# Kernel tuning notes

Measured on AMD Instinct MI355X. Metric: run time of the kernel, lower is better.

## Reference

```python
import jax, jax.numpy as jnp
import numpy as np

LN_EPS = 1e-12
NEG_INF = -1e9


def setup_inputs() -> dict:
    key = jax.random.key(0)
    ks = jax.random.split(key, 4)
    B, S, H = 8, 2048, 1024
    inputs = jax.random.normal(ks[0], (B, S, H), dtype=jnp.float32)
    masks = jnp.ones((B, S), dtype=jnp.int32)
    scale = 1.0 / np.sqrt(H)
    Wq = jax.random.normal(ks[1], (H, H), dtype=jnp.float32) * scale
    bq = jnp.zeros((H,), dtype=jnp.float32)
    Wk = jax.random.normal(ks[2], (H, H), dtype=jnp.float32) * scale
    bk = jnp.zeros((H,), dtype=jnp.float32)
    ln_gamma = jnp.ones((H,), dtype=jnp.float32)
    ln_beta = jnp.zeros((H,), dtype=jnp.float32)
    return {"inputs": inputs, "masks": masks, "Wq": Wq, "bq": bq,
            "Wk": Wk, "bk": bk, "ln_gamma": ln_gamma, "ln_beta": ln_beta}


def _layernorm(x, gamma, beta):
    mu = jnp.mean(x, axis=-1, keepdims=True)
    var = jnp.mean(jnp.square(x - mu), axis=-1, keepdims=True)
    return (x - mu) * jax.lax.rsqrt(var + LN_EPS) * gamma + beta


def reference(inputs, masks, Wq, bq, Wk, bk, ln_gamma, ln_beta):
    # inputs: [B,S,H]; masks: [B,S] (1 = keep key position)
    H = inputs.shape[-1]
    query = inputs @ Wq + bq                      # [B,S,H]
    key_ = inputs @ Wk + bk                       # [B,S,H]
    scores = jnp.einsum('bqh,bkh->bqk', query, key_) * (1.0 / jnp.sqrt(jnp.float32(H)))
    # logits_mask: invalid key positions get large negative logit
    scores = jnp.where(masks[:, None, :] != 0, scores, NEG_INF)
    probs = jax.nn.softmax(scores, axis=-1)       # [B,S,S]
    context = jnp.einsum('bqk,bkh->bqh', probs, inputs)  # value = raw inputs
    return _layernorm(inputs + context, ln_gamma, ln_beta)
```

## Files before the change

### kernel.cpp

```cpp
#include <hip/hip_runtime.h>
#include <stdint.h>
#include <stddef.h>

typedef _Float16 f16_t;
typedef _Float16 f16x8 __attribute__((ext_vector_type(8)));
typedef _Float16 f16x4 __attribute__((ext_vector_type(4)));
typedef float    f32x4 __attribute__((ext_vector_type(4)));

#define AS_G __attribute__((address_space(1)))
#define AS_L __attribute__((address_space(3)))

__device__ __forceinline__ void gload_lds16(const void* g, void* l) {
  __builtin_amdgcn_global_load_lds((const AS_G uint32_t*)g, (AS_L uint32_t*)l, 16, 0, 0);
}

#define LN_EPS 1e-12f

__global__ __launch_bounds__(256) void cast_f16_kernel(const float* __restrict__ in,
                                                       f16_t* __restrict__ out) {
  int i = blockIdx.x * 256 + threadIdx.x;
  float4 v = ((const float4*)in)[i];
  f16x4 o = {(f16_t)v.x, (f16_t)v.y, (f16_t)v.z, (f16_t)v.w};
  ((f16x4*)out)[i] = o;
}

__global__ __launch_bounds__(256) void xprep_kernel(const float* __restrict__ in,
                                                    f16_t* __restrict__ xb,
                                                    f16_t* __restrict__ xt) {
  __shared__ float tile[32][33];
  int b = blockIdx.z;
  const float* inb = in + (size_t)b * 2048 * 1024;
  f16_t* xbb = xb + (size_t)b * 2048 * 1024;
  f16_t* xtb = xt + (size_t)b * 1024 * 2048;
  int tx = threadIdx.x, ty = threadIdx.y;
  int c0 = blockIdx.x * 32, r0 = blockIdx.y * 32;
#pragma unroll
  for (int i = 0; i < 32; i += 8) {
    float v = inb[(size_t)(r0 + ty + i) * 1024 + (c0 + tx)];
    tile[ty + i][tx] = v;
    xbb[(size_t)(r0 + ty + i) * 1024 + (c0 + tx)] = (f16_t)v;
  }
  __syncthreads();
#pragma unroll
  for (int i = 0; i < 32; i += 8)
    xtb[(size_t)(c0 + ty + i) * 2048 + (r0 + tx)] = (f16_t)tile[tx][ty + i];
}

__global__ __launch_bounds__(256) void wvec_kernel(const float* __restrict__ Wq,
                                                   const float* __restrict__ bq,
                                                   const float* __restrict__ Wk,
                                                   const float* __restrict__ bk,
                                                   float* __restrict__ wqbk,
                                                   float* __restrict__ wkbq,
                                                   float* __restrict__ c0) {
  __shared__ float red[4];
  int bid = blockIdx.x, tid = threadIdx.x;
  const float* rowp; const float* vecp; float* outp;
  if (bid < 1024)      { rowp = Wq + (size_t)bid * 1024; vecp = bk; outp = wqbk + bid; }
  else if (bid < 2048) { rowp = Wk + (size_t)(bid - 1024) * 1024; vecp = bq; outp = wkbq + (bid - 1024); }
  else                 { rowp = bq; vecp = bk; outp = c0; }
  float4 a = ((const float4*)rowp)[tid];
  float4 b = ((const float4*)vecp)[tid];
  float s = a.x * b.x + a.y * b.y + a.z * b.z + a.w * b.w;
#pragma unroll
  for (int off = 32; off > 0; off >>= 1) s += __shfl_xor(s, off, 64);
  if ((tid & 63) == 0) red[tid >> 6] = s;
  __syncthreads();
  if (tid == 0) *outp = red[0] + red[1] + red[2] + red[3];
}

__global__ __launch_bounds__(256) void cqck_kernel(const float* __restrict__ X,
                                                   const float* __restrict__ wqbk,
                                                   const float* __restrict__ wkbq,
                                                   float* __restrict__ cq,
                                                   float* __restrict__ ck) {
  __shared__ float r1[4], r2[4];
  int m = blockIdx.x, tid = threadIdx.x;
  float4 x = ((const float4*)(X + (size_t)m * 1024))[tid];
  float4 a = ((const float4*)wqbk)[tid];
  float4 b = ((const float4*)wkbq)[tid];
  float s1 = x.x * a.x + x.y * a.y + x.z * a.z + x.w * a.w;
  float s2 = x.x * b.x + x.y * b.y + x.z * b.z + x.w * b.w;
#pragma unroll
  for (int off = 32; off > 0; off >>= 1) { s1 += __shfl_xor(s1, off, 64); s2 += __shfl_xor(s2, off, 64); }
  if ((tid & 63) == 0) { r1[tid >> 6] = s1; r2[tid >> 6] = s2; }
  __syncthreads();
  if (tid == 0) {
    cq[m] = r1[0] + r1[1] + r1[2] + r1[3];
    ck[m] = r2[0] + r2[1] + r2[2] + r2[3];
  }
}

__global__ __launch_bounds__(256) void gemm_bt_kernel(
    const f16_t* __restrict__ A, const f16_t* __restrict__ Bt, f16_t* __restrict__ C,
    const float* __restrict__ cq, const float* __restrict__ ck, const float* __restrict__ c0p,
    const int* __restrict__ mask, const float* __restrict__ invl, float* __restrict__ lpart,
    int lda, int ldb, int ldc, int K, float scale, int mode,
    size_t sA, size_t sB, size_t sC) {
  __shared__ f16_t As[2][128 * 64];
  __shared__ f16_t Bs[2][128 * 64];

  const int tid = threadIdx.x;
  const int lane = tid & 63;
  const int wv = tid >> 6;
  const int m16 = lane & 15;
  const int quad = lane >> 4;
  const int wr = (wv >> 1) * 64;
  const int wc = (wv & 1) * 64;

  const f16_t* Ab = A + blockIdx.z * sA + (size_t)blockIdx.x * 128 * lda;
  const f16_t* Bb = Bt + blockIdx.z * sB + (size_t)blockIdx.y * 128 * ldb;

  const int lr8 = lane >> 3;
  const int ch8 = (lane & 7) ^ lr8;
  const f16_t* gA[4]; const f16_t* gB[4];
  f16_t* lA[4]; f16_t* lB[4];
#pragma unroll
  for (int j = 0; j < 4; ++j) {
    int row = wv * 32 + j * 8 + lr8;
    gA[j] = Ab + (size_t)row * lda + ch8 * 8;
    gB[j] = Bb + (size_t)row * ldb + ch8 * 8;
    lA[j] = &As[0][(wv * 32 + j * 8) * 64];
    lB[j] = &Bs[0][(wv * 32 + j * 8) * 64];
  }

  int aoff[4], boff[4], swz[2];
#pragma unroll
  for (int t = 0; t < 4; ++t) {
    aoff[t] = (wr + t * 16 + m16) * 64;
    boff[t] = (wc + t * 16 + m16) * 64;
  }
#pragma unroll
  for (int s = 0; s < 2; ++s)
    swz[s] = (((s << 2) | quad) ^ (m16 & 7)) * 8;

  f32x4 acc[4][4] = {};

#define STAGE(BUF, KOFF)                                       \
  _Pragma("unroll")                                            \
  for (int j = 0; j < 4; ++j) {                                \
    gload_lds16(gA[j] + (KOFF), lA[j] + (BUF) * (128 * 64));   \
    gload_lds16(gB[j] + (KOFF), lB[j] + (BUF) * (128 * 64));   \
  }

#define COMPUTE(BUF)                                                           \
  _Pragma("unroll")                                                            \
  for (int s = 0; s < 2; ++s) {                                                \
    f16x8 af[4], bfr[4];                                                       \
    _Pragma("unroll")                                                          \
    for (int t = 0; t < 4; ++t) {                                              \
      af[t]  = *(const f16x8*)&As[BUF][aoff[t] + swz[s]];                      \
      bfr[t] = *(const f16x8*)&Bs[BUF][boff[t] + swz[s]];                      \
    }                                                                          \
    _Pragma("unroll")                                                          \
    for (int rt = 0; rt < 4; ++rt)                                             \
      _Pragma("unroll")                                                        \
      for (int ct = 0; ct < 4; ++ct)                                           \
        acc[rt][ct] = __builtin_amdgcn_mfma_f32_16x16x32_f16(af[rt], bfr[ct],  \
                                                             acc[rt][ct], 0, 0, 0); \
  }

  STAGE(0, 0);
  __syncthreads();

  for (int k0 = 0; k0 < K; k0 += 128) {
    STAGE(1, k0 + 64);
    COMPUTE(0);
    __syncthreads();
    if (k0 + 128 < K) STAGE(0, k0 + 128);
    COMPUTE(1);
    __syncthreads();
  }
#undef STAGE
#undef COMPUTE

  f16_t* Cb = C + blockIdx.z * sC;
  const int row0 = blockIdx.x * 128 + wr + quad * 4;
  const int col0 = blockIdx.y * 128 + wc + m16;
  if (mode == 0) {
#pragma unroll
    for (int ct = 0; ct < 4; ++ct)
#pragma unroll
      for (int rt = 0; rt < 4; ++rt)
#pragma unroll
        for (int r = 0; r < 4; ++r)
          Cb[(size_t)(row0 + rt * 16 + r) * ldc + col0 + ct * 16] = (f16_t)acc[rt][ct][r];
  } else if (mode == 1) {
    const int* mp = mask + blockIdx.z * 2048;
    const size_t rowg0 = blockIdx.z * 2048 + row0;
    const float c0 = *c0p;
    float rsum[4][4];
#pragma unroll
    for (int rt = 0; rt < 4; ++rt)
#pragma unroll
      for (int r = 0; r < 4; ++r) rsum[rt][r] = 0.f;
#pragma unroll
    for (int ct = 0; ct < 4; ++ct) {
      int col = col0 + ct * 16;
      bool keep = (mp[col] != 0);
      float ckv = ck[blockIdx.z * 2048 + col];
#pragma unroll
      for (int rt = 0; rt < 4; ++rt)
#pragma unroll
        for (int r = 0; r < 4; ++r) {
          float cqv = cq[rowg0 + rt * 16 + r];
          float p = keep ? __expf((acc[rt][ct][r] + cqv + ckv + c0) * scale) : 0.f;
          rsum[rt][r] += p;
          Cb[(size_t)(row0 + rt * 16 + r) * ldc + col] = (f16_t)p;
        }
    }
    const int chunk = blockIdx.y * 2 + (wv & 1);
#pragma unroll
    for (int rt = 0; rt < 4; ++rt)
#pragma unroll
      for (int r = 0; r < 4; ++r) {
        float v = rsum[rt][r];
        v += __shfl_xor(v, 1, 16);
        v += __shfl_xor(v, 2, 16);
        v += __shfl_xor(v, 4, 16);
        v += __shfl_xor(v, 8, 16);
        if (m16 == 0) lpart[(rowg0 + rt * 16 + r) * 32 + chunk] = v;
      }
  } else {
    const size_t rowg0 = blockIdx.z * 2048 + row0;
#pragma unroll
    for (int rt = 0; rt < 4; ++rt)
#pragma unroll
      for (int r = 0; r < 4; ++r) {
        float il = invl[rowg0 + rt * 16 + r];
#pragma unroll
        for (int ct = 0; ct < 4; ++ct)
          Cb[(size_t)(row0 + rt * 16 + r) * ldc + col0 + ct * 16] = (f16_t)(acc[rt][ct][r] * il);
      }
  }
}

__global__ __launch_bounds__(256) void lreduce_kernel(const float* __restrict__ lpart,
                                                      float* __restrict__ invl) {
  int m = blockIdx.x * 256 + threadIdx.x;
  const float4* p = (const float4*)(lpart + (size_t)m * 32);
  float s = 0.f;
#pragma unroll
  for (int j = 0; j < 8; ++j) {
    float4 v = p[j];
    s += v.x + v.y + v.z + v.w;
  }
  invl[m] = 1.0f / fmaxf(s, 1e-30f);
}

__global__ __launch_bounds__(256) void ln_kernel(const float* __restrict__ X,
                                                 const f16_t* __restrict__ Ctx,
                                                 const float* __restrict__ gamma,
                                                 const float* __restrict__ beta,
                                                 float* __restrict__ out) {
  __shared__ float r1[4], r2[4];
  const int tid = threadIdx.x;
  const size_t base = (size_t)blockIdx.x * 1024;
  float4 xv = ((const float4*)(X + base))[tid];
  f16x4 cv = ((const f16x4*)(Ctx + base))[tid];
  float v0 = xv.x + (float)cv[0];
  float v1 = xv.y + (float)cv[1];
  float v2 = xv.z + (float)cv[2];
  float v3 = xv.w + (float)cv[3];
  float s1 = v0 + v1 + v2 + v3;
  float s2 = v0 * v0 + v1 * v1 + v2 * v2 + v3 * v3;
#pragma unroll
  for (int off = 32; off > 0; off >>= 1) {
    s1 += __shfl_xor(s1, off, 64);
    s2 += __shfl_xor(s2, off, 64);
  }
  if ((tid & 63) == 0) { r1[tid >> 6] = s1; r2[tid >> 6] = s2; }
  __syncthreads();
  s1 = r1[0] + r1[1] + r1[2] + r1[3];
  s2 = r2[0] + r2[1] + r2[2] + r2[3];
  float mu = s1 * (1.0f / 1024.0f);
  float var = s2 * (1.0f / 1024.0f) - mu * mu;
  float rs = rsqrtf(fmaxf(var, 0.0f) + LN_EPS);
  float4 gv = ((const float4*)gamma)[tid];
  float4 bv = ((const float4*)beta)[tid];
  float4 o;
  o.x = (v0 - mu) * rs * gv.x + bv.x;
  o.y = (v1 - mu) * rs * gv.y + bv.y;
  o.z = (v2 - mu) * rs * gv.z + bv.z;
  o.w = (v3 - mu) * rs * gv.w + bv.w;
  ((float4*)(out + base))[tid] = o;
}

extern "C" void kernel_launch(void* const* d_in, const int* in_sizes, int n_in,
                              void* d_out, int out_size, void* d_ws, size_t ws_size,
                              hipStream_t stream) {
  const float* X     = (const float*)d_in[0];
  const int*   masks = (const int*)d_in[1];
  const float* Wq    = (const float*)d_in[2];
  const float* bq    = (const float*)d_in[3];
  const float* Wk    = (const float*)d_in[4];
  const float* bk    = (const float*)d_in[5];
  const float* gamma = (const float*)d_in[6];
  const float* beta  = (const float*)d_in[7];
  float* out = (float*)d_out;

  if (ws_size < 115343360u) return;
  char* ws = (char*)d_ws;
  f16_t* Xb   = (f16_t*)(ws + 0);
  f16_t* Xt   = (f16_t*)(ws + 33554432);
  f16_t* T    = (f16_t*)(ws + 67108864);
  f16_t* Wqf  = (f16_t*)(ws + 100663296);
  f16_t* Wkf  = (f16_t*)(ws + 102760448);
  f16_t* Wkq  = (f16_t*)(ws + 104857600);
  float* lpart= (float*)(ws + 106954752);
  float* cq   = (float*)(ws + 109051904);
  float* ck   = (float*)(ws + 109117440);
  float* invl = (float*)(ws + 109182976);
  float* wqbk = (float*)(ws + 109248512);
  float* wkbq = (float*)(ws + 109252608);
  float* c0   = (float*)(ws + 109256704);
  f16_t* Ctx  = Xb;
  f16_t* probs = (f16_t*)d_out;

  const size_t SH = 2048u * 1024u;
  const size_t SS = 2048u * 2048u;
  const size_t HS = 1024u * 2048u;

  xprep_kernel<<<dim3(32, 64, 8), dim3(32, 8), 0, stream>>>(X, Xb, Xt);
  cast_f16_kernel<<<1024, 256, 0, stream>>>(Wq, Wqf);
  cast_f16_kernel<<<1024, 256, 0, stream>>>(Wk, Wkf);
  wvec_kernel<<<2049, 256, 0, stream>>>(Wq, bq, Wk, bk, wqbk, wkbq, c0);
  cqck_kernel<<<16384, 256, 0, stream>>>(X, wqbk, wkbq, cq, ck);

  gemm_bt_kernel<<<dim3(8, 8, 1), 256, 0, stream>>>(
      Wkf, Wqf, Wkq, nullptr, nullptr, nullptr, nullptr, nullptr, nullptr,
      1024, 1024, 1024, 1024, 0.f, 0, 0, 0, 0);

  gemm_bt_kernel<<<dim3(128, 8, 1), 256, 0, stream>>>(
      Xb, Wkq, T, nullptr, nullptr, nullptr, nullptr, nullptr, nullptr,
      1024, 1024, 1024, 1024, 0.f, 0, 0, 0, 0);

  gemm_bt_kernel<<<dim3(16, 16, 8), 256, 0, stream>>>(
      T, Xb, probs, cq, ck, c0, masks, nullptr, lpart,
      1024, 1024, 2048, 1024, 0.03125f, 1, SH, SH, SS);

  lreduce_kernel<<<64, 256, 0, stream>>>(lpart, invl);

  gemm_bt_kernel<<<dim3(16, 8, 8), 256, 0, stream>>>(
      probs, Xt, Ctx, nullptr, nullptr, nullptr, nullptr, invl, nullptr,
      2048, 2048, 1024, 2048, 0.f, 2, SS, HS, SH);

  ln_kernel<<<16384, 256, 0, stream>>>(X, Ctx, gamma, beta, out);
}
```

Measured before the change: 471.6 us.

## Use 256x256 single-buffered 8-wave GEMM tiles for the large matmuls

Adds a 512-thread GEMM kernel with 256x256 output tiles, each wave computing 128x64, and routes the three large GEMMs (X·Wkq, the scores/softmax-numerator pass, and probs·X) through it. The larger tile doubles operand reuse per LDS load and halves global traffic per FLOP. In exchange it drops double buffering: one LDS stage per 64-wide K step with two barriers, so load latency is no longer hidden behind MFMA work. Higher register pressure from 32 accumulators per wave may also limit occupancy. The small weight GEMM keeps the old kernel, now with its unused epilogue arguments removed.

```diff
diff --git a/kernel.cpp b/kernel.cpp
--- a/kernel.cpp
+++ b/kernel.cpp
@@ -12,6 +12,12 @@
 
 __device__ __forceinline__ void gload_lds16(const void* g, void* l) {
   __builtin_amdgcn_global_load_lds((const AS_G uint32_t*)g, (AS_L uint32_t*)l, 16, 0, 0);
+}
+
+__device__ __forceinline__ void stage8(const f16_t* g, int ld, char* l) {
+#pragma unroll
+  for (int j = 0; j < 4; ++j)
+    gload_lds16(g + (size_t)(j * 8) * ld, l + j * 1024);
 }
 
 #define LN_EPS 1e-12f
@@ -93,10 +99,7 @@
 
 __global__ __launch_bounds__(256) void gemm_bt_kernel(
     const f16_t* __restrict__ A, const f16_t* __restrict__ Bt, f16_t* __restrict__ C,
-    const float* __restrict__ cq, const float* __restrict__ ck, const float* __restrict__ c0p,
-    const int* __restrict__ mask, const float* __restrict__ invl, float* __restrict__ lpart,
-    int lda, int ldb, int ldc, int K, float scale, int mode,
-    size_t sA, size_t sB, size_t sC) {
+    int lda, int ldb, int ldc, int K) {
   __shared__ f16_t As[2][128 * 64];
   __shared__ f16_t Bs[2][128 * 64];
 
@@ -108,8 +111,8 @@
   const int wr = (wv >> 1) * 64;
   const int wc = (wv & 1) * 64;
 
-  const f16_t* Ab = A + blockIdx.z * sA + (size_t)blockIdx.x * 128 * lda;
-  const f16_t* Bb = Bt + blockIdx.z * sB + (size_t)blockIdx.y * 128 * ldb;
+  const f16_t* Ab = A + (size_t)blockIdx.x * 128 * lda;
+  const f16_t* Bb = Bt + (size_t)blockIdx.y * 128 * ldb;
 
   const int lr8 = lane >> 3;
   const int ch8 = (lane & 7) ^ lr8;
@@ -162,7 +165,6 @@
 
   STAGE(0, 0);
   __syncthreads();
-
   for (int k0 = 0; k0 < K; k0 += 128) {
     STAGE(1, k0 + 64);
     COMPUTE(0);
@@ -174,63 +176,133 @@
 #undef STAGE
 #undef COMPUTE
 
-  f16_t* Cb = C + blockIdx.z * sC;
   const int row0 = blockIdx.x * 128 + wr + quad * 4;
   const int col0 = blockIdx.y * 128 + wc + m16;
+#pragma unroll
+  for (int ct = 0; ct < 4; ++ct)
+#pragma unroll
+    for (int rt = 0; rt < 4; ++rt)
+#pragma unroll
+      for (int r = 0; r < 4; ++r)
+        C[(size_t)(row0 + rt * 16 + r) * ldc + col0 + ct * 16] = (f16_t)acc[rt][ct][r];
+}
+
+__global__ __launch_bounds__(512) void gemm256_kernel(
+    const f16_t* __restrict__ A, const f16_t* __restrict__ Bt, f16_t* __restrict__ C,
+    const float* __restrict__ cq, const float* __restrict__ ck, const float* __restrict__ c0p,
+    const int* __restrict__ mask, const float* __restrict__ invl, float* __restrict__ lpart,
+    int lda, int ldb, int ldc, int K, float scale, int mode,
+    size_t sA, size_t sB, size_t sC) {
+  __shared__ f16_t As[256 * 64];
+  __shared__ f16_t Bs[256 * 64];
+
+  const int tid = threadIdx.x;
+  const int lane = tid & 63;
+  const int wid = tid >> 6;
+  const int wm = wid >> 2;
+  const int wn = wid & 3;
+  const int m16 = lane & 15;
+  const int quad = lane >> 4;
+
+  const f16_t* Ab = A + blockIdx.z * sA + (size_t)blockIdx.x * 256 * lda;
+  const f16_t* Bb = Bt + blockIdx.z * sB + (size_t)blockIdx.y * 256 * ldb;
+
+  const int lr8 = lane >> 3;
+  const int ch8 = (lane & 7) ^ lr8;
+  const f16_t* gA = Ab + (size_t)(wid * 32 + lr8) * lda + ch8 * 8;
+  const f16_t* gB = Bb + (size_t)(wid * 32 + lr8) * ldb + ch8 * 8;
+  char* ldsA = (char*)As + wid * 4096;
+  char* ldsB = (char*)Bs + wid * 4096;
+
+  int aoff[8], boff[4], swz[2];
+#pragma unroll
+  for (int mr = 0; mr < 8; ++mr) aoff[mr] = (wm * 128 + mr * 16 + m16) * 64;
+#pragma unroll
+  for (int nr = 0; nr < 4; ++nr) boff[nr] = (wn * 64 + nr * 16 + m16) * 64;
+#pragma unroll
+  for (int s = 0; s < 2; ++s)
+    swz[s] = (((s << 2) | quad) ^ (m16 & 7)) * 8;
+
+  f32x4 acc[8][4] = {};
+
+  for (int k0 = 0; k0 < K; k0 += 64) {
+    stage8(gA + k0, lda, ldsA);
+    stage8(gB + k0, ldb, ldsB);
+    __syncthreads();
+#pragma unroll
+    for (int s = 0; s < 2; ++s) {
+      f16x8 af[8], bf[4];
+#pragma unroll
+      for (int mr = 0; mr < 8; ++mr) af[mr] = *(const f16x8*)&As[aoff[mr] + swz[s]];
+#pragma unroll
+      for (int nr = 0; nr < 4; ++nr) bf[nr] = *(const f16x8*)&Bs[boff[nr] + swz[s]];
+#pragma unroll
+      for (int mr = 0; mr < 8; ++mr)
+#pragma unroll
+        for (int nr = 0; nr < 4; ++nr)
+          acc[mr][nr] = __builtin_amdgcn_mfma_f32_16x16x32_f16(af[mr], bf[nr],
+                                                               acc[mr][nr], 0, 0, 0);
+    }
+    __syncthreads();
+  }
+
+  f16_t* Cb = C + blockIdx.z * sC;
+  const int row0 = blockIdx.x * 256 + wm * 128 + quad * 4;
+  const int col0 = blockIdx.y * 256 + wn * 64 + m16;
   if (mode == 0) {
 #pragma unroll
-    for (int ct = 0; ct < 4; ++ct)
-#pragma unroll
-      for (int rt = 0; rt < 4; ++rt)
+    for (int nr = 0; nr < 4; ++nr)
+#pragma unroll
+      for (int mr = 0; mr < 8; ++mr)
 #pragma unroll
         for (int r = 0; r < 4; ++r)
-          Cb[(size_t)(row0 + rt * 16 + r) * ldc + col0 + ct * 16] = (f16_t)acc[rt][ct][r];
+          Cb[(size_t)(row0 + mr * 16 + r) * ldc + col0 + nr * 16] = (f16_t)acc[mr][nr][r];
   } else if (mode == 1) {
     const int* mp = mask + blockIdx.z * 2048;
     const size_t rowg0 = blockIdx.z * 2048 + row0;
     const float c0 = *c0p;
-    float rsum[4][4];
-#pragma unroll
-    for (int rt = 0; rt < 4; ++rt)
-#pragma unroll
-      for (int r = 0; r < 4; ++r) rsum[rt][r] = 0.f;
-#pragma unroll
-    for (int ct = 0; ct < 4; ++ct) {
-      int col = col0 + ct * 16;
+    float rsum[8][4];
+#pragma unroll
+    for (int mr = 0; mr < 8; ++mr)
+#pragma unroll
+      for (int r = 0; r < 4; ++r) rsum[mr][r] = 0.f;
+#pragma unroll
+    for (int nr = 0; nr < 4; ++nr) {
+      int col = col0 + nr * 16;
       bool keep = (mp[col] != 0);
       float ckv = ck[blockIdx.z * 2048 + col];
 #pragma unroll
-      for (int rt = 0; rt < 4; ++rt)
+      for (int mr = 0; mr < 8; ++mr)
 #pragma unroll
         for (int r = 0; r < 4; ++r) {
-          float cqv = cq[rowg0 + rt * 16 + r];
-          float p = keep ? __expf((acc[rt][ct][r] + cqv + ckv + c0) * scale) : 0.f;
-          rsum[rt][r] += p;
-          Cb[(size_t)(row0 + rt * 16 + r) * ldc + col] = (f16_t)p;
+          float cqv = cq[rowg0 + mr * 16 + r];
+          float p = keep ? __expf((acc[mr][nr][r] + cqv + ckv + c0) * scale) : 0.f;
+          rsum[mr][r] += p;
+          Cb[(size_t)(row0 + mr * 16 + r) * ldc + col] = (f16_t)p;
         }
     }
-    const int chunk = blockIdx.y * 2 + (wv & 1);
-#pragma unroll
-    for (int rt = 0; rt < 4; ++rt)
+    const int chunk = blockIdx.y * 4 + wn;
+#pragma unroll
+    for (int mr = 0; mr < 8; ++mr)
 #pragma unroll
       for (int r = 0; r < 4; ++r) {
-        float v = rsum[rt][r];
+        float v = rsum[mr][r];
         v += __shfl_xor(v, 1, 16);
         v += __shfl_xor(v, 2, 16);
         v += __shfl_xor(v, 4, 16);
         v += __shfl_xor(v, 8, 16);
-        if (m16 == 0) lpart[(rowg0 + rt * 16 + r) * 32 + chunk] = v;
+        if (m16 == 0) lpart[(rowg0 + mr * 16 + r) * 32 + chunk] = v;
       }
   } else {
     const size_t rowg0 = blockIdx.z * 2048 + row0;
 #pragma unroll
-    for (int rt = 0; rt < 4; ++rt)
+    for (int mr = 0; mr < 8; ++mr)
 #pragma unroll
       for (int r = 0; r < 4; ++r) {
-        float il = invl[rowg0 + rt * 16 + r];
-#pragma unroll
-        for (int ct = 0; ct < 4; ++ct)
-          Cb[(size_t)(row0 + rt * 16 + r) * ldc + col0 + ct * 16] = (f16_t)(acc[rt][ct][r] * il);
+        float il = invl[rowg0 + mr * 16 + r];
+#pragma unroll
+        for (int nr = 0; nr < 4; ++nr)
+          Cb[(size_t)(row0 + mr * 16 + r) * ldc + col0 + nr * 16] = (f16_t)(acc[mr][nr][r] * il);
       }
   }
 }
@@ -328,20 +400,19 @@
   cqck_kernel<<<16384, 256, 0, stream>>>(X, wqbk, wkbq, cq, ck);
 
   gemm_bt_kernel<<<dim3(8, 8, 1), 256, 0, stream>>>(
-      Wkf, Wqf, Wkq, nullptr, nullptr, nullptr, nullptr, nullptr, nullptr,
-      1024, 1024, 1024, 1024, 0.f, 0, 0, 0, 0);
-
-  gemm_bt_kernel<<<dim3(128, 8, 1), 256, 0, stream>>>(
+      Wkf, Wqf, Wkq, 1024, 1024, 1024, 1024);
+
+  gemm256_kernel<<<dim3(64, 4, 1), 512, 0, stream>>>(
       Xb, Wkq, T, nullptr, nullptr, nullptr, nullptr, nullptr, nullptr,
       1024, 1024, 1024, 1024, 0.f, 0, 0, 0, 0);
 
-  gemm_bt_kernel<<<dim3(16, 16, 8), 256, 0, stream>>>(
+  gemm256_kernel<<<dim3(8, 8, 8), 512, 0, stream>>>(
       T, Xb, probs, cq, ck, c0, masks, nullptr, lpart,
       1024, 1024, 2048, 1024, 0.03125f, 1, SH, SH, SS);
 
   lreduce_kernel<<<64, 256, 0, stream>>>(lpart, invl);
 
-  gemm_bt_kernel<<<dim3(16, 8, 8), 256, 0, stream>>>(
+  gemm256_kernel<<<dim3(8, 4, 8), 512, 0, stream>>>(
       probs, Xt, Ctx, nullptr, nullptr, nullptr, nullptr, invl, nullptr,
       2048, 2048, 1024, 2048, 0.f, 2, SS, HS, SH);
 
```

After: 490.9 us. 1.04x slower.
